# Kernel optimization log

Measured on AMD Instinct MI355X. Metric: run time of the kernel, lower is better.

## Reference

```python
import jax, jax.numpy as jnp
import numpy as np

N, E, F, H = 50000, 800000, 128, 128

def silu(v):
    return v * jax.nn.sigmoid(v)

def setup_inputs() -> dict:
    key = jax.random.key(0)
    ks = jax.random.split(key, 16)
    def lin(k, fan_in, fan_out):
        s = 1.0 / np.sqrt(fan_in)
        kw, kb = jax.random.split(k)
        W = jax.random.uniform(kw, (fan_in, fan_out), jnp.float32, -s, s)
        b = jax.random.uniform(kb, (fan_out,), jnp.float32, -s, s)
        return W, b
    x = jax.random.normal(ks[0], (N, F), jnp.float32)
    pos = jax.random.normal(ks[1], (N, 3), jnp.float32)
    edge_index = jax.random.randint(ks[2], (2, E), 0, N, jnp.int64)
    We1, be1 = lin(ks[3], 2 * F + 1, H)
    We2, be2 = lin(ks[4], H, H)
    Wn1, bn1 = lin(ks[5], F + H, H)
    Wn2, bn2 = lin(ks[6], H, F)
    Wc, bc = lin(ks[7], H, 1)
    return {"x": x, "pos": pos, "We1": We1, "be1": be1, "We2": We2, "be2": be2,
            "Wn1": Wn1, "bn1": bn1, "Wn2": Wn2, "bn2": bn2, "Wc": Wc, "bc": bc,
            "edge_index": edge_index}

def reference(x, pos, We1, be1, We2, be2, Wn1, bn1, Wn2, bn2, Wc, bc, edge_index):
    row, col = edge_index[0], edge_index[1]
    rij = pos[row] - pos[col]                      # [E,3]
    dij = jnp.sum(rij ** 2, axis=-1, keepdims=True)  # [E,1]
    edge_input = jnp.concatenate([x[row], x[col], dij], axis=-1)  # [E,2F+1]
    m_ij = silu(silu(edge_input @ We1 + be1) @ We2 + be2)          # [E,H]
    agg = jax.ops.segment_sum(m_ij, row, num_segments=N)          # [N,H]
    x_new = silu(jnp.concatenate([x, agg], axis=-1) @ Wn1 + bn1) @ Wn2 + bn2  # [N,F]
    w_ij = silu(m_ij @ Wc + bc)                    # [E,1]
    trans = rij * w_ij                             # [E,3]
    delta = jax.ops.segment_sum(trans, row, num_segments=N)       # [N,3]
    pos_new = pos + 0.01 * delta
    return (x_new, pos_new)
```

## Files before the change

### kernel.cpp

```cpp
#include <hip/hip_runtime.h>
#include <hip/hip_bf16.h>
#include <stdint.h>
#include <string.h>

#define NN 50000
#define NE 800000
#define SCAN_B 200
#define SCAN_CH 250

typedef short bf8_t __attribute__((ext_vector_type(8)));
typedef float f32x4 __attribute__((ext_vector_type(4)));

__device__ __forceinline__ float silu_f(float v) {
    return v * __builtin_amdgcn_rcpf(1.0f + __expf(-v));
}

__device__ __forceinline__ unsigned int pack2bf(float a, float b) {
    __hip_bfloat162 h = __float22bfloat162_rn(make_float2(a, b));
    unsigned int u; memcpy(&u, &h, 4);
    return u;
}

__device__ __forceinline__ float bf_lo(unsigned int u) { return __uint_as_float(u << 16); }
__device__ __forceinline__ float bf_hi(unsigned int u) { return __uint_as_float(u & 0xffff0000u); }

union U4B { uint4 u; bf8_t b; };
__device__ __forceinline__ bf8_t as_bf8(uint4 u) { U4B x; x.u = u; return x.b; }

__global__ __launch_bounds__(256) void prep_x_hist(const float* __restrict__ x,
                                                   unsigned short* __restrict__ xbf,
                                                   const int* __restrict__ ei,
                                                   int* __restrict__ cnt) {
    size_t i = (size_t)blockIdx.x * 256 + threadIdx.x;
    const float4* s = (const float4*)(x + i * 8);
    float4 v0 = s[0], v1 = s[1];
    uint4 o;
    o.x = pack2bf(v0.x, v0.y); o.y = pack2bf(v0.z, v0.w);
    o.z = pack2bf(v1.x, v1.y); o.w = pack2bf(v1.z, v1.w);
    *(uint4*)(xbf + i * 8) = o;
    atomicAdd(&cnt[ei[i]], 1);
}

__global__ __launch_bounds__(64) void prep_w(const float* __restrict__ We1,
                                             const float* __restrict__ We2,
                                             const float* __restrict__ Wn1,
                                             const float* __restrict__ Wn2,
                                             unsigned short* __restrict__ wf1,
                                             unsigned short* __restrict__ wf2,
                                             unsigned short* __restrict__ wfn1,
                                             unsigned short* __restrict__ wfn2) {
    int b = blockIdx.x, lane = threadIdx.x;
    int q = lane >> 4, c = lane & 15;
    const float* W; unsigned short* dst; int f;
    if (b < 64)       { W = We1; f = b;       dst = wf1  + (size_t)f * 512; }
    else if (b < 96)  { W = We2; f = b - 64;  dst = wf2  + (size_t)f * 512; }
    else if (b < 160) { W = Wn1; f = b - 96;  dst = wfn1 + (size_t)f * 512; }
    else              { W = Wn2; f = b - 160; dst = wfn2 + (size_t)f * 512; }
    int s = f >> 3, mf = f & 7;
    int k0 = s * 32 + q * 8, col = mf * 16 + c;
    float v[8];
    #pragma unroll
    for (int i = 0; i < 8; ++i) v[i] = W[(size_t)(k0 + i) * 128 + col];
    uint4 o;
    o.x = pack2bf(v[0], v[1]); o.y = pack2bf(v[2], v[3]);
    o.z = pack2bf(v[4], v[5]); o.w = pack2bf(v[6], v[7]);
    *(uint4*)(dst + lane * 8) = o;
}

__global__ __launch_bounds__(256, 4) void prep_zy(
    const unsigned short* __restrict__ xbf, const unsigned short* __restrict__ wf1,
    const float* __restrict__ be1,
    unsigned short* __restrict__ zbf, unsigned short* __restrict__ ybf)
{
    const int tid = threadIdx.x;
    const int n0 = blockIdx.x * 64;
    const char* xb = (const char*)xbf;
    const char* w1 = (const char*)wf1;

    const int P = tid >> 6, lane = tid & 63;
    const int q = lane >> 4, e16 = lane & 15;
    const int oc_q = P * 32 + q * 4;

    int nloc[4]; unsigned nb[4];
    #pragma unroll
    for (int t = 0; t < 4; ++t) {
        int nl = t * 16 + e16; nloc[t] = nl;
        int node = n0 + nl; if (node >= NN) node = NN - 1;
        nb[t] = (unsigned)node;
    }

    f32x4 accz[2][4], accy[2][4];
    #pragma unroll
    for (int M = 0; M < 2; ++M) {
        float4 bi = *(const float4*)(be1 + oc_q + M * 16);
        #pragma unroll
        for (int t = 0; t < 4; ++t) {
            accz[M][t][0] = bi.x; accz[M][t][1] = bi.y; accz[M][t][2] = bi.z; accz[M][t][3] = bi.w;
            accy[M][t][0] = 0.f;  accy[M][t][1] = 0.f;  accy[M][t][2] = 0.f;  accy[M][t][3] = 0.f;
        }
    }

    #pragma unroll
    for (int s = 0; s < 4; ++s) {
        bf8_t bfr[4];
        #pragma unroll
        for (int t = 0; t < 4; ++t) {
            unsigned noff = (nb[t] << 8) + (unsigned)(s * 64 + q * 16);
            bfr[t] = as_bf8(*(const uint4*)(xb + noff));
        }
        #pragma unroll
        for (int M = 0; M < 2; ++M) {
            unsigned wz = ((unsigned)(s * 8 + P * 2 + M) << 10) + ((unsigned)lane << 4);
            unsigned wy = ((unsigned)((s + 4) * 8 + P * 2 + M) << 10) + ((unsigned)lane << 4);
            bf8_t afz = as_bf8(*(const uint4*)(w1 + wz));
            bf8_t afy = as_bf8(*(const uint4*)(w1 + wy));
            #pragma unroll
            for (int t = 0; t < 4; ++t) {
                accz[M][t] = __builtin_amdgcn_mfma_f32_16x16x32_bf16(afz, bfr[t], accz[M][t], 0, 0, 0);
                accy[M][t] = __builtin_amdgcn_mfma_f32_16x16x32_bf16(afy, bfr[t], accy[M][t], 0, 0, 0);
            }
        }
    }

    #pragma unroll
    for (int M = 0; M < 2; ++M) {
        #pragma unroll
        for (int t = 0; t < 4; ++t) {
            int node = n0 + nloc[t];
            if (node < NN) {
                uint2 pz, py;
                pz.x = pack2bf(accz[M][t][0], accz[M][t][1]);
                pz.y = pack2bf(accz[M][t][2], accz[M][t][3]);
                py.x = pack2bf(accy[M][t][0], accy[M][t][1]);
                py.y = pack2bf(accy[M][t][2], accy[M][t][3]);
                *(uint2*)(zbf + ((size_t)node << 7) + oc_q + M * 16) = pz;
                *(uint2*)(ybf + ((size_t)node << 7) + oc_q + M * 16) = py;
            }
        }
    }
}

__global__ __launch_bounds__(256) void scan_bsum(const int* __restrict__ cnt,
                                                 int* __restrict__ bsum) {
    __shared__ int red[4];
    int b = blockIdx.x, tid = threadIdx.x;
    int n = b * SCAN_CH + tid;
    int v = (tid < SCAN_CH) ? cnt[n] : 0;
    #pragma unroll
    for (int o = 32; o; o >>= 1) v += __shfl_down(v, o);
    if ((tid & 63) == 0) red[tid >> 6] = v;
    __syncthreads();
    if (tid == 0) bsum[b] = red[0] + red[1] + red[2] + red[3];
}

__global__ __launch_bounds__(256) void scan_write(const int* __restrict__ cnt,
                                                  const int* __restrict__ bsum,
                                                  int* __restrict__ off,
                                                  int* __restrict__ cur) {
    __shared__ int part[256];
    __shared__ int basered[4];
    int b = blockIdx.x, tid = threadIdx.x;
    int bv = (tid < b) ? bsum[tid] : 0;
    #pragma unroll
    for (int o = 32; o; o >>= 1) bv += __shfl_down(bv, o);
    if ((tid & 63) == 0) basered[tid >> 6] = bv;
    __syncthreads();
    int base = basered[0] + basered[1] + basered[2] + basered[3];
    int n = b * SCAN_CH + tid;
    int c = (tid < SCAN_CH) ? cnt[n] : 0;
    part[tid] = c;
    __syncthreads();
    #pragma unroll
    for (int d = 1; d < 256; d <<= 1) {
        int v = (tid >= d) ? part[tid - d] : 0;
        __syncthreads();
        part[tid] += v;
        __syncthreads();
    }
    if (tid < SCAN_CH) {
        int excl = base + part[tid] - c;
        off[n] = excl; cur[n] = excl;
    }
    if (b == SCAN_B - 1 && tid == SCAN_CH) off[NN] = NE;
}

__global__ __launch_bounds__(256) void egnn_scatter(const int* __restrict__ ei,
                                                    int* __restrict__ cur,
                                                    int2* __restrict__ rc_slot) {
    int e = blockIdx.x * 256 + threadIdx.x;
    if (e < NE) {
        int r = ei[e];
        int p = atomicAdd(&cur[r], 1);
        rc_slot[p] = make_int2(r, ei[NE + e]);
    }
}

__global__ __launch_bounds__(256, 4) void egnn_edge_mfma(
    const unsigned short* __restrict__ zbf, const unsigned short* __restrict__ ybf,
    const float* __restrict__ pos,
    const unsigned short* __restrict__ wf2,
    const float* __restrict__ We1,
    const float* __restrict__ be2, const float* __restrict__ Wc,
    const float* __restrict__ bc,
    const int2* __restrict__ rc_slot,
    float* __restrict__ agg, float* __restrict__ delta)
{
    __shared__ __align__(16) unsigned short HsBuf[9216];
    unsigned short* Hs = HsBuf;
    unsigned short* mT = HsBuf;
    __shared__ __align__(16) unsigned short Ss[64 * 72];
    __shared__ int   rows_s[64], cols_s[64];
    __shared__ float rij_s[64][3];
    __shared__ float dij_s[64];
    __shared__ float wdot[64];
    __shared__ int   seg_node[64], seg_start[64];
    __shared__ unsigned long long smask;
    __shared__ int firstPartial, lastPartial;

    const int tid = threadIdx.x;
    const int e0 = blockIdx.x * 64;
    const char* zb = (const char*)zbf;
    const char* yb = (const char*)ybf;
    const char* w2 = (const char*)wf2;

    if (tid < 64) {
        int2 rc = rc_slot[e0 + tid];
        rows_s[tid] = rc.x; cols_s[tid] = rc.y;
        float d = 0.f;
        #pragma unroll
        for (int k = 0; k < 3; ++k) {
            float rv = pos[rc.x * 3 + k] - pos[rc.y * 3 + k];
            rij_s[tid][k] = rv; d += rv * rv;
        }
        dij_s[tid] = d;
        wdot[tid] = 0.f;
    }
    __syncthreads();

    const int P = tid >> 6, lane = tid & 63;
    const int q = lane >> 4, e16 = lane & 15;
    const int oc_q = P * 32 + q * 4;

    int eloc[4]; unsigned rb[4], cb[4];
    #pragma unroll
    for (int t = 0; t < 4; ++t) {
        int el = t * 16 + e16; eloc[t] = el;
        rb[t] = (unsigned)rows_s[el] << 8;
        cb[t] = (unsigned)cols_s[el] << 8;
    }

    #pragma unroll
    for (int M = 0; M < 2; ++M) {
        const unsigned cbyte = (unsigned)((oc_q + M * 16) << 1);
        float4 w256 = *(const float4*)(We1 + (size_t)256 * 128 + oc_q + M * 16);
        #pragma unroll
        for (int t = 0; t < 4; ++t) {
            uint2 uz = *(const uint2*)(zb + rb[t] + cbyte);
            uint2 uy = *(const uint2*)(yb + cb[t] + cbyte);
            float d = dij_s[eloc[t]];
            float v0 = silu_f(bf_lo(uz.x) + bf_lo(uy.x) + d * w256.x);
            float v1 = silu_f(bf_hi(uz.x) + bf_hi(uy.x) + d * w256.y);
            float v2 = silu_f(bf_lo(uz.y) + bf_lo(uy.y) + d * w256.z);
            float v3 = silu_f(bf_hi(uz.y) + bf_hi(uy.y) + d * w256.w);
            uint2 pk; pk.x = pack2bf(v0, v1); pk.y = pack2bf(v2, v3);
            *(uint2*)(Hs + eloc[t] * 136 + oc_q + M * 16) = pk;
        }
    }
    __syncthreads();

    f32x4 acc2[2][4];
    #pragma unroll
    for (int M = 0; M < 2; ++M) {
        float4 bi = *(const float4*)(be2 + oc_q + M * 16);
        #pragma unroll
        for (int t = 0; t < 4; ++t) { acc2[M][t][0] = bi.x; acc2[M][t][1] = bi.y; acc2[M][t][2] = bi.z; acc2[M][t][3] = bi.w; }
    }

    #pragma unroll
    for (int s = 0; s < 4; ++s) {
        bf8_t bfr[4];
        #pragma unroll
        for (int t = 0; t < 4; ++t)
            bfr[t] = as_bf8(*(const uint4*)(Hs + eloc[t] * 136 + s * 32 + q * 8));
        __builtin_amdgcn_s_setprio(1);
        #pragma unroll
        for (int M = 0; M < 2; ++M) {
            unsigned woff = ((unsigned)(s * 8 + P * 2 + M) << 10) + ((unsigned)lane << 4);
            bf8_t af = as_bf8(*(const uint4*)(w2 + woff));
            #pragma unroll
            for (int t = 0; t < 4; ++t)
                acc2[M][t] = __builtin_amdgcn_mfma_f32_16x16x32_bf16(af, bfr[t], acc2[M][t], 0, 0, 0);
        }
        __builtin_amdgcn_s_setprio(0);
    }
    __syncthreads();

    {
        unsigned int* S32 = (unsigned int*)Ss;
        #pragma unroll
        for (int i = tid; i < 64 * 72 / 2; i += 256) S32[i] = 0;
    }
    {
        float4 wcA = *(const float4*)(Wc + oc_q);
        float4 wcB = *(const float4*)(Wc + oc_q + 16);
        float part[4];
        #pragma unroll
        for (int t = 0; t < 4; ++t) part[t] = 0.f;

        #pragma unroll
        for (int M = 0; M < 2; ++M) {
            float4 wc = (M == 0) ? wcA : wcB;
            int cbase = oc_q + M * 16;
            #pragma unroll
            for (int t = 0; t < 4; ++t) {
                float v0 = silu_f(acc2[M][t][0]);
                float v1 = silu_f(acc2[M][t][1]);
                float v2 = silu_f(acc2[M][t][2]);
                float v3 = silu_f(acc2[M][t][3]);
                part[t] += v0 * wc.x + v1 * wc.y + v2 * wc.z + v3 * wc.w;
                unsigned ua = pack2bf(v0, v1), ub = pack2bf(v2, v3);
                int slot = eloc[t];
                mT[(cbase + 0) * 72 + slot] = (unsigned short)ua;
                mT[(cbase + 1) * 72 + slot] = (unsigned short)(ua >> 16);
                mT[(cbase + 2) * 72 + slot] = (unsigned short)ub;
                mT[(cbase + 3) * 72 + slot] = (unsigned short)(ub >> 16);
            }
        }
        #pragma unroll
        for (int t = 0; t < 4; ++t) {
            float p = part[t];
            p += __shfl_xor(p, 16);
            p += __shfl_xor(p, 32);
            if (q == 0) atomicAdd(&wdot[eloc[t]], p);
        }
    }
    __syncthreads();

    if (tid < 64) {
        float wgt = silu_f(wdot[tid] + bc[0]);
        rij_s[tid][0] *= wgt; rij_s[tid][1] *= wgt; rij_s[tid][2] *= wgt;
        bool flag = (tid == 0) || (rows_s[tid] != rows_s[tid - 1]);
        unsigned long long b = __ballot(flag);
        int seg = __popcll(b & ((2ull << tid) - 1)) - 1;
        Ss[seg * 72 + tid] = 0x3F80;
        if (flag) { seg_node[seg] = rows_s[tid]; seg_start[seg] = tid; }
        if (tid == 0) {
            smask = b;
            firstPartial = (e0 > 0) && (rc_slot[e0 - 1].x == rows_s[0]);
            lastPartial  = (e0 + 64 < NE) && (rc_slot[e0 + 64].x == rows_s[63]);
        }
    }
    __syncthreads();

    {
        const int wv = tid >> 6, l = tid & 63;
        const int cA = l & 15, kq = l >> 4;
        const int nseg = __popcll(smask);
        f32x4 accd[8];
        #pragma unroll
        for (int ct = 0; ct < 8; ++ct) { accd[ct][0] = 0.f; accd[ct][1] = 0.f; accd[ct][2] = 0.f; accd[ct][3] = 0.f; }
        #pragma unroll
        for (int kt = 0; kt < 2; ++kt) {
            bf8_t aS = as_bf8(*(const uint4*)(Ss + (wv * 16 + cA) * 72 + kt * 32 + kq * 8));
            #pragma unroll
            for (int ct = 0; ct < 8; ++ct) {
                bf8_t bM = as_bf8(*(const uint4*)(mT + (ct * 16 + cA) * 72 + kt * 32 + kq * 8));
                accd[ct] = __builtin_amdgcn_mfma_f32_16x16x32_bf16(aS, bM, accd[ct], 0, 0, 0);
            }
        }
        #pragma unroll
        for (int ct = 0; ct < 8; ++ct) {
            #pragma unroll
            for (int r = 0; r < 4; ++r) {
                int seg = wv * 16 + kq * 4 + r;
                if (seg < nseg) {
                    float v = accd[ct][r];
                    int node = seg_node[seg];
                    bool partial = (seg == 0 && firstPartial) || (seg == nseg - 1 && lastPartial);
                    float* dst = agg + (size_t)node * 128 + ct * 16 + cA;
                    if (partial) atomicAdd(dst, v); else *dst = v;
                }
            }
        }
        if (tid < 64 && tid < nseg) {
            int start = seg_start[tid];
            int end = (tid + 1 < nseg) ? seg_start[tid + 1] : 64;
            float d0 = 0.f, d1 = 0.f, d2 = 0.f;
            for (int s2 = start; s2 < end; ++s2) {
                d0 += rij_s[s2][0]; d1 += rij_s[s2][1]; d2 += rij_s[s2][2];
            }
            int node = seg_node[tid];
            bool partial = (tid == 0 && firstPartial) || (tid == nseg - 1 && lastPartial);
            float* dd = delta + (size_t)node * 3;
            if (partial) { atomicAdd(dd, d0); atomicAdd(dd + 1, d1); atomicAdd(dd + 2, d2); }
            else         { dd[0] = d0; dd[1] = d1; dd[2] = d2; }
        }
    }
}

__global__ __launch_bounds__(256, 4) void egnn_node_mfma(
    const unsigned short* __restrict__ xbf, const float* __restrict__ agg,
    const float* __restrict__ delta, const float* __restrict__ pos,
    const unsigned short* __restrict__ wfn1, const unsigned short* __restrict__ wfn2,
    const float* __restrict__ bn1, const float* __restrict__ bn2,
    float* __restrict__ out)
{
    __shared__ unsigned short Hs[64 * 136];

    const int tid = threadIdx.x;
    const int n0 = blockIdx.x * 64;
    const char* xb = (const char*)xbf;
    const char* ab = (const char*)agg;
    const char* w1 = (const char*)wfn1;
    const char* w2 = (const char*)wfn2;

    if (tid < 192) {
        int n = n0 + tid / 3, d = tid - 3 * (tid / 3);
        if (n < NN)
            out[(size_t)NN * 128 + (size_t)n * 3 + d] =
                pos[(size_t)n * 3 + d] + 0.01f * delta[(size_t)n * 3 + d];
    }

    const int P = tid >> 6, lane = tid & 63;
    const int q = lane >> 4, e16 = lane & 15;
    const int oc_q = P * 32 + q * 4;

    int nloc[4]; unsigned nb[4];
    #pragma unroll
    for (int t = 0; t < 4; ++t) {
        int nl = t * 16 + e16; nloc[t] = nl;
        int node = n0 + nl; if (node >= NN) node = NN - 1;
        nb[t] = (unsigned)node;
    }

    f32x4 acc[2][4];
    #pragma unroll
    for (int M = 0; M < 2; ++M) {
        float4 bi = *(const float4*)(bn1 + oc_q + M * 16);
        #pragma unroll
        for (int t = 0; t < 4; ++t) { acc[M][t][0] = bi.x; acc[M][t][1] = bi.y; acc[M][t][2] = bi.z; acc[M][t][3] = bi.w; }
    }

    #pragma unroll
    for (int s = 0; s < 8; ++s) {
        bf8_t bfr[4];
        #pragma unroll
        for (int t = 0; t < 4; ++t) {
            if (s < 4) {
                unsigned noff = (nb[t] << 8) + (unsigned)((s & 3) * 64 + q * 16);
                bfr[t] = as_bf8(*(const uint4*)(xb + noff));
            } else {
                unsigned aoff = (nb[t] << 9) + (unsigned)(((s & 3) * 32 + q * 8) * 4);
                float4 a0 = *(const float4*)(ab + aoff);
                float4 a1 = *(const float4*)(ab + aoff + 16);
                uint4 o;
                o.x = pack2bf(a0.x, a0.y); o.y = pack2bf(a0.z, a0.w);
                o.z = pack2bf(a1.x, a1.y); o.w = pack2bf(a1.z, a1.w);
                bfr[t] = as_bf8(o);
            }
        }
        #pragma unroll
        for (int M = 0; M < 2; ++M) {
            unsigned woff = ((unsigned)(s * 8 + P * 2 + M) << 10) + ((unsigned)lane << 4);
            bf8_t af = as_bf8(*(const uint4*)(w1 + woff));
            #pragma unroll
            for (int t = 0; t < 4; ++t)
                acc[M][t] = __builtin_amdgcn_mfma_f32_16x16x32_bf16(af, bfr[t], acc[M][t], 0, 0, 0);
        }
    }

    #pragma unroll
    for (int M = 0; M < 2; ++M) {
        #pragma unroll
        for (int t = 0; t < 4; ++t) {
            float v0 = silu_f(acc[M][t][0]);
            float v1 = silu_f(acc[M][t][1]);
            float v2 = silu_f(acc[M][t][2]);
            float v3 = silu_f(acc[M][t][3]);
            uint2 pk; pk.x = pack2bf(v0, v1); pk.y = pack2bf(v2, v3);
            *(uint2*)(Hs + nloc[t] * 136 + oc_q + M * 16) = pk;
        }
    }
    __syncthreads();

    f32x4 acc2[2][4];
    #pragma unroll
    for (int M = 0; M < 2; ++M) {
        float4 bi = *(const float4*)(bn2 + oc_q + M * 16);
        #pragma unroll
        for (int t = 0; t < 4; ++t) { acc2[M][t][0] = bi.x; acc2[M][t][1] = bi.y; acc2[M][t][2] = bi.z; acc2[M][t][3] = bi.w; }
    }

    #pragma unroll
    for (int s = 0; s < 4; ++s) {
        bf8_t bfr[4];
        #pragma unroll
        for (int t = 0; t < 4; ++t)
            bfr[t] = as_bf8(*(const uint4*)(Hs + nloc[t] * 136 + s * 32 + q * 8));
        #pragma unroll
        for (int M = 0; M < 2; ++M) {
            unsigned woff = ((unsigned)(s * 8 + P * 2 + M) << 10) + ((unsigned)lane << 4);
            bf8_t af = as_bf8(*(const uint4*)(w2 + woff));
            #pragma unroll
            for (int t = 0; t < 4; ++t)
                acc2[M][t] = __builtin_amdgcn_mfma_f32_16x16x32_bf16(af, bfr[t], acc2[M][t], 0, 0, 0);
        }
    }

    #pragma unroll
    for (int M = 0; M < 2; ++M) {
        #pragma unroll
        for (int t = 0; t < 4; ++t) {
            int node = n0 + nloc[t];
            if (node < NN) {
                float4 v; v.x = acc2[M][t][0]; v.y = acc2[M][t][1]; v.z = acc2[M][t][2]; v.w = acc2[M][t][3];
                *(float4*)(out + (size_t)node * 128 + oc_q + M * 16) = v;
            }
        }
    }
}

extern "C" void kernel_launch(void* const* d_in, const int* in_sizes, int n_in,
                              void* d_out, int out_size, void* d_ws, size_t ws_size,
                              hipStream_t stream)
{
    const float* x   = (const float*)d_in[0];
    const float* pos = (const float*)d_in[1];
    const float* We1 = (const float*)d_in[2];
    const float* be1 = (const float*)d_in[3];
    const float* We2 = (const float*)d_in[4];
    const float* be2 = (const float*)d_in[5];
    const float* Wn1 = (const float*)d_in[6];
    const float* bn1 = (const float*)d_in[7];
    const float* Wn2 = (const float*)d_in[8];
    const float* bn2 = (const float*)d_in[9];
    const float* Wc  = (const float*)d_in[10];
    const float* bc  = (const float*)d_in[11];
    const int*   ei  = (const int*)d_in[12];
    float* out = (float*)d_out;

    char* p = (char*)d_ws;
    float* agg   = (float*)p;                  p += (size_t)NN * 128 * 4;
    float* delta = (float*)p;                  p += (size_t)NN * 3 * 4;
    int* cnt     = (int*)p;                    p += (size_t)NN * 4;
    unsigned short* xbf = (unsigned short*)p;  p += (size_t)NN * 128 * 2;
    unsigned short* zbf = (unsigned short*)p;  p += (size_t)NN * 128 * 2;
    unsigned short* ybf = (unsigned short*)p;  p += (size_t)NN * 128 * 2;
    unsigned short* wf1  = (unsigned short*)p; p += 65536;
    unsigned short* wf2  = (unsigned short*)p; p += 32768;
    unsigned short* wfn1 = (unsigned short*)p; p += 65536;
    unsigned short* wfn2 = (unsigned short*)p; p += 32768;
    int* off   = (int*)p;                      p += (size_t)(NN + 1) * 4 + 12;
    int* cur   = (int*)p;                      p += (size_t)NN * 4;
    int* bsum  = (int*)p;                      p += (size_t)SCAN_B * 4;
    int2* rc_slot = (int2*)p;

    hipMemsetAsync(agg, 0, ((size_t)NN * 128 + (size_t)NN * 3 + NN) * 4, stream);

    prep_x_hist<<<3125, 256, 0, stream>>>(x, xbf, ei, cnt);
    prep_w<<<192, 64, 0, stream>>>(We1, We2, Wn1, Wn2, wf1, wf2, wfn1, wfn2);
    prep_zy<<<(NN + 63) / 64, 256, 0, stream>>>(xbf, wf1, be1, zbf, ybf);
    scan_bsum<<<SCAN_B, 256, 0, stream>>>(cnt, bsum);
    scan_write<<<SCAN_B, 256, 0, stream>>>(cnt, bsum, off, cur);
    egnn_scatter<<<NE / 256, 256, 0, stream>>>(ei, cur, rc_slot);
    egnn_edge_mfma<<<NE / 64, 256, 0, stream>>>(zbf, ybf, pos, wf2, We1, be2,
                                                Wc, bc, rc_slot, agg, delta);
    egnn_node_mfma<<<(NN + 63) / 64, 256, 0, stream>>>(xbf, agg, delta, pos,
                                                       wfn1, wfn2, bn1, bn2, out);
}
```

Measured before the change: 310.7 us.

## Fuse x conversion and degree histogram into node prep; trim edge kernel LDS

Folds the bf16 conversion of x and the row-degree histogram into the per-node prep kernel, which now reads fp32 x directly for its MFMA operands. This removes one kernel launch and a dependent round trip through xbf. In the edge kernel, the z/y gathers are issued before the first barrier, cols_s is dropped, and the segment-indicator matrix is built in registers from seg_start instead of being zeroed and written into a shared Ss buffer. This lowers LDS use and barrier-bound latency, at the cost of extra register pressure and repeated fp32 loads of x.

```diff
diff --git a/kernel.cpp b/kernel.cpp
--- a/kernel.cpp
+++ b/kernel.cpp
@@ -26,20 +26,6 @@
 
 union U4B { uint4 u; bf8_t b; };
 __device__ __forceinline__ bf8_t as_bf8(uint4 u) { U4B x; x.u = u; return x.b; }
-
-__global__ __launch_bounds__(256) void prep_x_hist(const float* __restrict__ x,
-                                                   unsigned short* __restrict__ xbf,
-                                                   const int* __restrict__ ei,
-                                                   int* __restrict__ cnt) {
-    size_t i = (size_t)blockIdx.x * 256 + threadIdx.x;
-    const float4* s = (const float4*)(x + i * 8);
-    float4 v0 = s[0], v1 = s[1];
-    uint4 o;
-    o.x = pack2bf(v0.x, v0.y); o.y = pack2bf(v0.z, v0.w);
-    o.z = pack2bf(v1.x, v1.y); o.w = pack2bf(v1.z, v1.w);
-    *(uint4*)(xbf + i * 8) = o;
-    atomicAdd(&cnt[ei[i]], 1);
-}
 
 __global__ __launch_bounds__(64) void prep_w(const float* __restrict__ We1,
                                              const float* __restrict__ We2,
@@ -67,15 +53,41 @@
     *(uint4*)(dst + lane * 8) = o;
 }
 
-__global__ __launch_bounds__(256, 4) void prep_zy(
-    const unsigned short* __restrict__ xbf, const unsigned short* __restrict__ wf1,
-    const float* __restrict__ be1,
-    unsigned short* __restrict__ zbf, unsigned short* __restrict__ ybf)
+__global__ __launch_bounds__(256, 4) void prep_node(
+    const float* __restrict__ x, const int* __restrict__ ei,
+    const unsigned short* __restrict__ wf1, const float* __restrict__ be1,
+    unsigned short* __restrict__ xbf, unsigned short* __restrict__ zbf,
+    unsigned short* __restrict__ ybf, int* __restrict__ cnt)
 {
     const int tid = threadIdx.x;
     const int n0 = blockIdx.x * 64;
-    const char* xb = (const char*)xbf;
     const char* w1 = (const char*)wf1;
+
+    {
+        int e0 = (blockIdx.x * 256 + tid) * 4;
+        if (e0 < NE) {
+            int4 r4 = *(const int4*)(ei + e0);
+            atomicAdd(&cnt[r4.x], 1); atomicAdd(&cnt[r4.y], 1);
+            atomicAdd(&cnt[r4.z], 1); atomicAdd(&cnt[r4.w], 1);
+        }
+    }
+
+    {
+        int node = n0 + (tid >> 2);
+        if (node < NN) {
+            const float* src = x + (size_t)node * 128 + (tid & 3) * 32;
+            unsigned short* dst = xbf + (size_t)node * 128 + (tid & 3) * 32;
+            #pragma unroll
+            for (int j = 0; j < 4; ++j) {
+                float4 v0 = *(const float4*)(src + j * 8);
+                float4 v1 = *(const float4*)(src + j * 8 + 4);
+                uint4 o;
+                o.x = pack2bf(v0.x, v0.y); o.y = pack2bf(v0.z, v0.w);
+                o.z = pack2bf(v1.x, v1.y); o.w = pack2bf(v1.z, v1.w);
+                *(uint4*)(dst + j * 8) = o;
+            }
+        }
+    }
 
     const int P = tid >> 6, lane = tid & 63;
     const int q = lane >> 4, e16 = lane & 15;
@@ -105,8 +117,13 @@
         bf8_t bfr[4];
         #pragma unroll
         for (int t = 0; t < 4; ++t) {
-            unsigned noff = (nb[t] << 8) + (unsigned)(s * 64 + q * 16);
-            bfr[t] = as_bf8(*(const uint4*)(xb + noff));
+            const float* src = x + ((size_t)nb[t]) * 128 + s * 32 + q * 8;
+            float4 v0 = *(const float4*)src;
+            float4 v1 = *(const float4*)(src + 4);
+            uint4 o;
+            o.x = pack2bf(v0.x, v0.y); o.y = pack2bf(v0.z, v0.w);
+            o.z = pack2bf(v1.x, v1.y); o.w = pack2bf(v1.z, v1.w);
+            bfr[t] = as_bf8(o);
         }
         #pragma unroll
         for (int M = 0; M < 2; ++M) {
@@ -208,8 +225,7 @@
     __shared__ __align__(16) unsigned short HsBuf[9216];
     unsigned short* Hs = HsBuf;
     unsigned short* mT = HsBuf;
-    __shared__ __align__(16) unsigned short Ss[64 * 72];
-    __shared__ int   rows_s[64], cols_s[64];
+    __shared__ int   rows_s[64];
     __shared__ float rij_s[64][3];
     __shared__ float dij_s[64];
     __shared__ float wdot[64];
@@ -225,7 +241,7 @@
 
     if (tid < 64) {
         int2 rc = rc_slot[e0 + tid];
-        rows_s[tid] = rc.x; cols_s[tid] = rc.y;
+        rows_s[tid] = rc.x;
         float d = 0.f;
         #pragma unroll
         for (int k = 0; k < 3; ++k) {
@@ -234,8 +250,8 @@
         }
         dij_s[tid] = d;
         wdot[tid] = 0.f;
-    }
-    __syncthreads();
+        seg_start[tid] = 64;
+    }
 
     const int P = tid >> 6, lane = tid & 63;
     const int q = lane >> 4, e16 = lane & 15;
@@ -245,18 +261,29 @@
     #pragma unroll
     for (int t = 0; t < 4; ++t) {
         int el = t * 16 + e16; eloc[t] = el;
-        rb[t] = (unsigned)rows_s[el] << 8;
-        cb[t] = (unsigned)cols_s[el] << 8;
-    }
-
+        int2 rc = rc_slot[e0 + el];
+        rb[t] = (unsigned)rc.x << 8;
+        cb[t] = (unsigned)rc.y << 8;
+    }
+
+    uint2 uzr[2][4], uyr[2][4];
     #pragma unroll
     for (int M = 0; M < 2; ++M) {
         const unsigned cbyte = (unsigned)((oc_q + M * 16) << 1);
+        #pragma unroll
+        for (int t = 0; t < 4; ++t) {
+            uzr[M][t] = *(const uint2*)(zb + rb[t] + cbyte);
+            uyr[M][t] = *(const uint2*)(yb + cb[t] + cbyte);
+        }
+    }
+    __syncthreads();
+
+    #pragma unroll
+    for (int M = 0; M < 2; ++M) {
         float4 w256 = *(const float4*)(We1 + (size_t)256 * 128 + oc_q + M * 16);
         #pragma unroll
         for (int t = 0; t < 4; ++t) {
-            uint2 uz = *(const uint2*)(zb + rb[t] + cbyte);
-            uint2 uy = *(const uint2*)(yb + cb[t] + cbyte);
+            uint2 uz = uzr[M][t], uy = uyr[M][t];
             float d = dij_s[eloc[t]];
             float v0 = silu_f(bf_lo(uz.x) + bf_lo(uy.x) + d * w256.x);
             float v1 = silu_f(bf_hi(uz.x) + bf_hi(uy.x) + d * w256.y);
@@ -295,11 +322,6 @@
     }
     __syncthreads();
 
-    {
-        unsigned int* S32 = (unsigned int*)Ss;
-        #pragma unroll
-        for (int i = tid; i < 64 * 72 / 2; i += 256) S32[i] = 0;
-    }
     {
         float4 wcA = *(const float4*)(Wc + oc_q);
         float4 wcB = *(const float4*)(Wc + oc_q + 16);
@@ -342,7 +364,6 @@
         bool flag = (tid == 0) || (rows_s[tid] != rows_s[tid - 1]);
         unsigned long long b = __ballot(flag);
         int seg = __popcll(b & ((2ull << tid) - 1)) - 1;
-        Ss[seg * 72 + tid] = 0x3F80;
         if (flag) { seg_node[seg] = rows_s[tid]; seg_start[seg] = tid; }
         if (tid == 0) {
             smask = b;
@@ -356,12 +377,20 @@
         const int wv = tid >> 6, l = tid & 63;
         const int cA = l & 15, kq = l >> 4;
         const int nseg = __popcll(smask);
+        const int seg = wv * 16 + cA;
+        const int st = seg_start[seg];
+        const int en = (seg < 63) ? seg_start[seg + 1] : 64;
         f32x4 accd[8];
         #pragma unroll
         for (int ct = 0; ct < 8; ++ct) { accd[ct][0] = 0.f; accd[ct][1] = 0.f; accd[ct][2] = 0.f; accd[ct][3] = 0.f; }
         #pragma unroll
         for (int kt = 0; kt < 2; ++kt) {
-            bf8_t aS = as_bf8(*(const uint4*)(Ss + (wv * 16 + cA) * 72 + kt * 32 + kq * 8));
+            bf8_t aS;
+            #pragma unroll
+            for (int i = 0; i < 8; ++i) {
+                int k = kt * 32 + kq * 8 + i;
+                aS[i] = (k >= st && k < en) ? (short)0x3F80 : (short)0;
+            }
             #pragma unroll
             for (int ct = 0; ct < 8; ++ct) {
                 bf8_t bM = as_bf8(*(const uint4*)(mT + (ct * 16 + cA) * 72 + kt * 32 + kq * 8));
@@ -372,11 +401,11 @@
         for (int ct = 0; ct < 8; ++ct) {
             #pragma unroll
             for (int r = 0; r < 4; ++r) {
-                int seg = wv * 16 + kq * 4 + r;
-                if (seg < nseg) {
+                int sg = wv * 16 + kq * 4 + r;
+                if (sg < nseg) {
                     float v = accd[ct][r];
-                    int node = seg_node[seg];
-                    bool partial = (seg == 0 && firstPartial) || (seg == nseg - 1 && lastPartial);
+                    int node = seg_node[sg];
+                    bool partial = (sg == 0 && firstPartial) || (sg == nseg - 1 && lastPartial);
                     float* dst = agg + (size_t)node * 128 + ct * 16 + cA;
                     if (partial) atomicAdd(dst, v); else *dst = v;
                 }
@@ -557,9 +586,8 @@
 
     hipMemsetAsync(agg, 0, ((size_t)NN * 128 + (size_t)NN * 3 + NN) * 4, stream);
 
-    prep_x_hist<<<3125, 256, 0, stream>>>(x, xbf, ei, cnt);
     prep_w<<<192, 64, 0, stream>>>(We1, We2, Wn1, Wn2, wf1, wf2, wfn1, wfn2);
-    prep_zy<<<(NN + 63) / 64, 256, 0, stream>>>(xbf, wf1, be1, zbf, ybf);
+    prep_node<<<(NN + 63) / 64, 256, 0, stream>>>(x, ei, wf1, be1, xbf, zbf, ybf, cnt);
     scan_bsum<<<SCAN_B, 256, 0, stream>>>(cnt, bsum);
     scan_write<<<SCAN_B, 256, 0, stream>>>(cnt, bsum, off, cur);
     egnn_scatter<<<NE / 256, 256, 0, stream>>>(ei, cur, rc_slot);
```

Result: no change. 307.2 us (-1.1%).
